# Kernel tuning notes

Hardware: AMD Instinct MI355X
Metric: run time of the kernel (lower is better)

Reference implementation:

```python
import jax, jax.numpy as jnp
import numpy as np

B, C, H, W = 8, 1, 512, 512


def _unwrap(p, axis=-2):
    # Faithful jnp port of np.unwrap (default discont=pi, period=2*pi)
    pi = jnp.pi
    d = jnp.diff(p, axis=axis)
    dd = jnp.mod(d + pi, 2.0 * pi) - pi
    dd = jnp.where((dd == -pi) & (d > 0), pi, dd)
    corr = dd - d
    corr = jnp.where(jnp.abs(d) < pi, 0.0, corr)
    cum = jnp.cumsum(corr, axis=axis)
    pad_cfg = [(0, 0)] * p.ndim
    pad_cfg[axis] = (1, 0)
    return p + jnp.pad(cum, pad_cfg)


def _conv_same(x, w, b, dil):
    # PyTorch padding='same': total = dil*(k-1), left = total//2, right = rest
    th = dil * (w.shape[2] - 1)
    tw = dil * (w.shape[3] - 1)
    pad = [(th // 2, th - th // 2), (tw // 2, tw - tw // 2)]
    y = jax.lax.conv_general_dilated(
        x, w, window_strides=(1, 1), padding=pad,
        rhs_dilation=(dil, dil),
        dimension_numbers=('NCHW', 'OIHW', 'NCHW'))
    return y + b[None, :, None, None]


def setup_inputs() -> dict:
    key = jax.random.key(0)
    ks = jax.random.split(key, 9)
    s = 0.05
    return {
        'feature_in': jax.random.normal(ks[0], (B, C, H, W), dtype=jnp.float32),
        'w1': jax.random.normal(ks[1], (2, 1, 4, 4), dtype=jnp.float32) * s,
        'b1': jax.random.normal(ks[2], (2,), dtype=jnp.float32) * s,
        'w2': jax.random.normal(ks[3], (4, 3, 3, 3), dtype=jnp.float32) * s,
        'b2': jax.random.normal(ks[4], (4,), dtype=jnp.float32) * s,
        'w3': jax.random.normal(ks[5], (8, 8, 2, 2), dtype=jnp.float32) * s,
        'b3': jax.random.normal(ks[6], (8,), dtype=jnp.float32) * s,
        'w4': jax.random.normal(ks[7], (16, 20, 1, 1), dtype=jnp.float32) * s,
        'b4': jax.random.normal(ks[8], (16,), dtype=jnp.float32) * s,
    }


def reference(feature_in, w1, b1, w2, b2, w3, b3, w4, b4):
    out = _unwrap(feature_in, axis=-2)
    diff = out[:, :, 1:, :] - out[:, :, :-1, :]           # [B,C,H-1,W]
    padded = jnp.pad(diff, ((0, 0), (0, 0), (1, 0), (0, 0)))  # pad top of H
    sq = padded * padded                                   # [B,1,H,W]
    o1 = _conv_same(sq, w1, b1, 1)
    o1 = jnp.concatenate((o1, sq), axis=1)                 # 3 ch
    o2 = _conv_same(o1, w2, b2, 2)
    o2 = jnp.concatenate((o2, o1, sq), axis=1)             # 8 ch
    o3 = _conv_same(o2, w3, b3, 3)
    o3 = jnp.concatenate((o3, o2, o1, sq), axis=1)         # 20 ch
    o4 = _conv_same(o3, w4, b4, 4)
    o4 = jnp.concatenate((o4, o3, o2, o1, sq), axis=1)     # 48 ch
    return o4
```

## Files before the change

### kernel.cpp

```cpp
#include <hip/hip_runtime.h>

#define HH 512
#define WW 512
#define TS 32
#define SQH 42
#define SQW 42
#define O1H 39
#define O1W 39
#define O2H 35
#define O2W 35

#define W2T 0
#define W3T 108
#define W4T 332
#define B2O 572
#define B3O 576
#define B4O 584

__global__ void prep_weights(const float* __restrict__ w2, const float* __restrict__ b2,
                             const float* __restrict__ w3, const float* __restrict__ b3,
                             const float* __restrict__ w4, const float* __restrict__ b4,
                             float* __restrict__ ws)
{
    int t = threadIdx.x;
    if (t < 108) {
        int c = t & 3, ci = (t >> 2) % 3, tap = t / 12;
        int i = tap / 3, j = tap % 3;
        ws[W2T + t] = w2[((c*3+ci)*3+i)*3+j];
    }
    if (t < 224) {
        int c = t & 7, ci = (t >> 3) % 7, tap = t / 56;
        int i = tap >> 1, j = tap & 1;
        float v = w3[((c*8+ci)*2+i)*2+j];
        if (ci == 6) v += w3[((c*8+7)*2+i)*2+j];
        ws[W3T + t] = v;
    }
    if (t < 240) {
        int c = t & 15, u = t >> 4;
        float v;
        if (u < 12)       v = w4[c*20+u];
        else if (u == 12) v = w4[c*20+12] + w4[c*20+16];
        else if (u == 13) v = w4[c*20+13] + w4[c*20+17];
        else              v = w4[c*20+14] + w4[c*20+15] + w4[c*20+18] + w4[c*20+19];
        ws[W4T + t] = v;
    }
    if (t < 4)  ws[B2O + t] = b2[t];
    if (t < 8)  ws[B3O + t] = b3[t];
    if (t < 16) ws[B4O + t] = b4[t];
}

__global__ __launch_bounds__(256) void enc_fused(
    const float* __restrict__ f,
    const float* __restrict__ w1, const float* __restrict__ b1,
    const float* __restrict__ wf,
    float* __restrict__ out)
{
    __shared__ __align__(16) float s_sq[SQH*SQW];
    __shared__ __align__(16) float s_o1[O1H*O1W*2];
    __shared__ __align__(16) float s_o2[O2H*O2W*4];

    const int tid = threadIdx.x;
    const int b  = blockIdx.z;
    const int h0 = blockIdx.y * TS;
    const int w0 = blockIdx.x * TS;

    const float* fb = f + (size_t)b * (HH*WW);
    const float PI = 3.14159265358979323846f;
    const float TWO_PI = 6.283185307179586477f;
    #pragma unroll
    for (int p = 0; p < 7; ++p) {
        int idx = tid + 256*p;
        if (idx < SQH*SQW) {
            int rh = idx / SQW, rw = idx % SQW;
            int gh = h0 + rh - 4, gw = w0 + rw - 4;
            float v = 0.f;
            if (gh > 0 && gh < HH && gw >= 0 && gw < WW) {
                float d = fb[gh*WW + gw] - fb[(gh-1)*WW + gw];
                float m = fmodf(d + PI, TWO_PI);
                if (m < 0.f) m += TWO_PI;
                float dd = m - PI;
                if (dd == -PI && d > 0.f) dd = PI;
                float r = (fabsf(d) < PI) ? d : dd;
                v = r * r;
            }
            s_sq[idx] = v;
        }
    }
    __syncthreads();

    #pragma unroll
    for (int p = 0; p < 6; ++p) {
        int idx = tid + 256*p;
        if (idx < O1H*O1W) {
            int rh = idx / O1W, rw = idx % O1W;
            float a0 = b1[0], a1 = b1[1];
            #pragma unroll
            for (int i = 0; i < 4; ++i)
            #pragma unroll
            for (int j = 0; j < 4; ++j) {
                float x = s_sq[(rh+i)*SQW + rw+j];
                a0 += x * w1[i*4+j];
                a1 += x * w1[16+i*4+j];
            }
            int gy = h0 + rh - 3, gx = w0 + rw - 3;
            bool inimg = (gy >= 0) & (gy < HH) & (gx >= 0) & (gx < WW);
            float2 o; o.x = inimg ? a0 : 0.f; o.y = inimg ? a1 : 0.f;
            *(float2*)&s_o1[idx*2] = o;
        }
    }
    __syncthreads();

    {
        int rh[5], rw[5]; bool val[5], img[5];
        float acc[4][5];
        #pragma unroll
        for (int p = 0; p < 5; ++p) {
            int idx = tid + 256*p;
            val[p] = idx < O2H*O2W;
            int id = val[p] ? idx : 0;
            rh[p] = id / O2W; rw[p] = id % O2W;
            int gy = h0 + rh[p] - 1, gx = w0 + rw[p] - 1;
            img[p] = (gy >= 0) & (gy < HH) & (gx >= 0) & (gx < WW);
            #pragma unroll
            for (int c = 0; c < 4; ++c) acc[c][p] = wf[B2O + c];
        }
        #pragma unroll
        for (int i = 0; i < 3; ++i)
        #pragma unroll
        for (int j = 0; j < 3; ++j) {
            const float4 wa = *(const float4*)&wf[W2T + (i*3+j)*12];
            const float4 wb = *(const float4*)&wf[W2T + (i*3+j)*12 + 4];
            const float4 wc = *(const float4*)&wf[W2T + (i*3+j)*12 + 8];
            #pragma unroll
            for (int p = 0; p < 5; ++p) {
                float2 xo = *(const float2*)&s_o1[((rh[p]+2*i)*O1W + rw[p]+2*j)*2];
                float  xs = s_sq[(rh[p]+1+2*i)*SQW + rw[p]+1+2*j];
                acc[0][p] += xo.x*wa.x + xo.y*wb.x + xs*wc.x;
                acc[1][p] += xo.x*wa.y + xo.y*wb.y + xs*wc.y;
                acc[2][p] += xo.x*wa.z + xo.y*wb.z + xs*wc.z;
                acc[3][p] += xo.x*wa.w + xo.y*wb.w + xs*wc.w;
            }
        }
        #pragma unroll
        for (int p = 0; p < 5; ++p) if (val[p]) {
            float4 o;
            o.x = img[p] ? acc[0][p] : 0.f;
            o.y = img[p] ? acc[1][p] : 0.f;
            o.z = img[p] ? acc[2][p] : 0.f;
            o.w = img[p] ? acc[3][p] : 0.f;
            *(float4*)&s_o2[(rh[p]*O2W + rw[p])*4] = o;
        }
    }
    __syncthreads();

    {
        const int rw = tid & 31;
        const int q  = tid >> 5;
        float sqv[4], o1v[2][4], o2v[4][4], o3v[8][4];
        #pragma unroll
        for (int k = 0; k < 4; ++k) {
            int rh = q + 8*k;
            sqv[k] = s_sq[(rh+4)*SQW + rw+4];
            float2 t2 = *(const float2*)&s_o1[((rh+3)*O1W + rw+3)*2];
            o1v[0][k]=t2.x; o1v[1][k]=t2.y;
            float4 t4 = *(const float4*)&s_o2[((rh+1)*O2W + rw+1)*4];
            o2v[0][k]=t4.x; o2v[1][k]=t4.y; o2v[2][k]=t4.z; o2v[3][k]=t4.w;
        }

        const size_t HWp = (size_t)HH*WW;
        float* ob = out + (size_t)b*48*HWp;
        int pofs[4];
        #pragma unroll
        for (int k = 0; k < 4; ++k) pofs[k] = (h0 + q + 8*k)*WW + (w0 + rw);

        #pragma unroll
        for (int k = 0; k < 4; ++k) {
            float* o = ob + pofs[k];
            #pragma unroll
            for (int c = 0; c < 4; ++c) o[(size_t)(24+c)*HWp] = o2v[c][k];
            o[28*HWp]=o1v[0][k]; o[29*HWp]=o1v[1][k]; o[30*HWp]=sqv[k]; o[31*HWp]=sqv[k];
            o[32*HWp]=o1v[0][k]; o[33*HWp]=o1v[1][k]; o[34*HWp]=sqv[k]; o[35*HWp]=sqv[k];
            #pragma unroll
            for (int c = 0; c < 4; ++c) o[(size_t)(36+c)*HWp] = o2v[c][k];
            o[40*HWp]=o1v[0][k]; o[41*HWp]=o1v[1][k]; o[42*HWp]=sqv[k]; o[43*HWp]=sqv[k];
            o[44*HWp]=o1v[0][k]; o[45*HWp]=o1v[1][k]; o[46*HWp]=sqv[k]; o[47*HWp]=sqv[k];
        }

        #pragma unroll
        for (int c = 0; c < 8; ++c) {
            float bv = wf[B3O + c];
            #pragma unroll
            for (int k = 0; k < 4; ++k) o3v[c][k] = bv;
        }
        #pragma unroll
        for (int i = 0; i < 2; ++i)
        #pragma unroll
        for (int j = 0; j < 2; ++j) {
            float xin[7][4];
            #pragma unroll
            for (int k = 0; k < 4; ++k) {
                int hh = q + 8*k + 3*i, ww = rw + 3*j;
                float4 a = *(const float4*)&s_o2[(hh*O2W+ww)*4];
                xin[0][k]=a.x; xin[1][k]=a.y; xin[2][k]=a.z; xin[3][k]=a.w;
                float2 bq = *(const float2*)&s_o1[((hh+2)*O1W + ww+2)*2];
                xin[4][k]=bq.x; xin[5][k]=bq.y;
                xin[6][k]=s_sq[(hh+3)*SQW + ww+3];
            }
            #pragma unroll
            for (int ci = 0; ci < 7; ++ci) {
                float4 wa = *(const float4*)&wf[W3T + (i*2+j)*56 + ci*8];
                float4 wb = *(const float4*)&wf[W3T + (i*2+j)*56 + ci*8 + 4];
                #pragma unroll
                for (int k = 0; k < 4; ++k) {
                    float x = xin[ci][k];
                    o3v[0][k] += x*wa.x; o3v[1][k] += x*wa.y;
                    o3v[2][k] += x*wa.z; o3v[3][k] += x*wa.w;
                    o3v[4][k] += x*wb.x; o3v[5][k] += x*wb.y;
                    o3v[6][k] += x*wb.z; o3v[7][k] += x*wb.w;
                }
            }
        }
        #pragma unroll
        for (int k = 0; k < 4; ++k) {
            float* o = ob + pofs[k];
            #pragma unroll
            for (int c = 0; c < 8; ++c) o[(size_t)(16+c)*HWp] = o3v[c][k];
        }

        #pragma unroll
        for (int cg = 0; cg < 4; ++cg) {
            float acc[4][4];
            #pragma unroll
            for (int c = 0; c < 4; ++c) {
                float bv = wf[B4O + cg*4 + c];
                #pragma unroll
                for (int k = 0; k < 4; ++k) acc[c][k] = bv;
            }
            #pragma unroll
            for (int u = 0; u < 15; ++u) {
                float4 wv = *(const float4*)&wf[W4T + u*16 + cg*4];
                #pragma unroll
                for (int k = 0; k < 4; ++k) {
                    float x = (u<8) ? o3v[u][k] : (u<12) ? o2v[u-8][k]
                            : (u<14) ? o1v[u-12][k] : sqv[k];
                    acc[0][k]+=x*wv.x; acc[1][k]+=x*wv.y;
                    acc[2][k]+=x*wv.z; acc[3][k]+=x*wv.w;
                }
            }
            #pragma unroll
            for (int c = 0; c < 4; ++c)
            #pragma unroll
            for (int k = 0; k < 4; ++k)
                ob[(size_t)(cg*4+c)*HWp + pofs[k]] = acc[c][k];
        }
    }
}

extern "C" void kernel_launch(void* const* d_in, const int* in_sizes, int n_in,
                              void* d_out, int out_size, void* d_ws, size_t ws_size,
                              hipStream_t stream) {
    const float* f  = (const float*)d_in[0];
    const float* w1 = (const float*)d_in[1];
    const float* b1 = (const float*)d_in[2];
    const float* w2 = (const float*)d_in[3];
    const float* b2 = (const float*)d_in[4];
    const float* w3 = (const float*)d_in[5];
    const float* b3 = (const float*)d_in[6];
    const float* w4 = (const float*)d_in[7];
    const float* b4 = (const float*)d_in[8];
    float* out = (float*)d_out;
    float* ws  = (float*)d_ws;

    prep_weights<<<1, 256, 0, stream>>>(w2, b2, w3, b3, w4, b4, ws);
    dim3 grid(WW/TS, HH/TS, 8);
    enc_fused<<<grid, 256, 0, stream>>>(f, w1, b1, ws, out);
}
```

Baseline: 100.4 us.

## Interleave global output stores with compute stages and replace fmodf with floor-based wrap

Output writes for the pass-through sq, o1 and o2 channels now happen right after each stage is computed, before the next barrier, not all at the end. The intent is to spread the large store traffic across the kernel so memory writes overlap with the later conv stages. The phase-wrap fmodf is replaced by an fma with floorf and a reciprocal of two pi, which is cheaper but can differ from fmodf by rounding near the wrap boundaries. Keeping sqv and o1v live across stages may raise register pressure.

```diff
diff --git a/kernel.cpp b/kernel.cpp
--- a/kernel.cpp
+++ b/kernel.cpp
@@ -64,21 +64,28 @@
     const int h0 = blockIdx.y * TS;
     const int w0 = blockIdx.x * TS;
 
+    const int rw = tid & 31;
+    const int q  = tid >> 5;
+    const size_t HWp = (size_t)HH*WW;
+    float* ob = out + (size_t)b*48*HWp;
+    int pofs[4];
+    #pragma unroll
+    for (int k = 0; k < 4; ++k) pofs[k] = (h0 + q + 8*k)*WW + (w0 + rw);
+
     const float* fb = f + (size_t)b * (HH*WW);
     const float PI = 3.14159265358979323846f;
     const float TWO_PI = 6.283185307179586477f;
+    const float INV2PI = 0.15915494309189533577f;
     #pragma unroll
     for (int p = 0; p < 7; ++p) {
         int idx = tid + 256*p;
         if (idx < SQH*SQW) {
-            int rh = idx / SQW, rw = idx % SQW;
-            int gh = h0 + rh - 4, gw = w0 + rw - 4;
+            int rh = idx / SQW, rwp = idx % SQW;
+            int gh = h0 + rh - 4, gw = w0 + rwp - 4;
             float v = 0.f;
             if (gh > 0 && gh < HH && gw >= 0 && gw < WW) {
                 float d = fb[gh*WW + gw] - fb[(gh-1)*WW + gw];
-                float m = fmodf(d + PI, TWO_PI);
-                if (m < 0.f) m += TWO_PI;
-                float dd = m - PI;
+                float dd = fmaf(-TWO_PI, floorf((d + PI) * INV2PI), d);
                 if (dd == -PI && d > 0.f) dd = PI;
                 float r = (fabsf(d) < PI) ? d : dd;
                 v = r * r;
@@ -88,38 +95,56 @@
     }
     __syncthreads();
 
+    float sqv[4];
+    #pragma unroll
+    for (int k = 0; k < 4; ++k) sqv[k] = s_sq[(q + 8*k + 4)*SQW + rw + 4];
+
     #pragma unroll
     for (int p = 0; p < 6; ++p) {
         int idx = tid + 256*p;
         if (idx < O1H*O1W) {
-            int rh = idx / O1W, rw = idx % O1W;
+            int rh = idx / O1W, rwp = idx % O1W;
             float a0 = b1[0], a1 = b1[1];
             #pragma unroll
             for (int i = 0; i < 4; ++i)
             #pragma unroll
             for (int j = 0; j < 4; ++j) {
-                float x = s_sq[(rh+i)*SQW + rw+j];
+                float x = s_sq[(rh+i)*SQW + rwp+j];
                 a0 += x * w1[i*4+j];
                 a1 += x * w1[16+i*4+j];
             }
-            int gy = h0 + rh - 3, gx = w0 + rw - 3;
+            int gy = h0 + rh - 3, gx = w0 + rwp - 3;
             bool inimg = (gy >= 0) & (gy < HH) & (gx >= 0) & (gx < WW);
             float2 o; o.x = inimg ? a0 : 0.f; o.y = inimg ? a1 : 0.f;
             *(float2*)&s_o1[idx*2] = o;
         }
     }
+    #pragma unroll
+    for (int k = 0; k < 4; ++k) {
+        float* o = ob + pofs[k];
+        float v = sqv[k];
+        o[30*HWp]=v; o[31*HWp]=v; o[34*HWp]=v; o[35*HWp]=v;
+        o[42*HWp]=v; o[43*HWp]=v; o[46*HWp]=v; o[47*HWp]=v;
+    }
     __syncthreads();
 
+    float o1v[2][4];
+    #pragma unroll
+    for (int k = 0; k < 4; ++k) {
+        float2 t2 = *(const float2*)&s_o1[((q + 8*k + 3)*O1W + rw + 3)*2];
+        o1v[0][k]=t2.x; o1v[1][k]=t2.y;
+    }
+
     {
-        int rh[5], rw[5]; bool val[5], img[5];
+        int rh[5], rwp[5]; bool val[5], img[5];
         float acc[4][5];
         #pragma unroll
         for (int p = 0; p < 5; ++p) {
             int idx = tid + 256*p;
             val[p] = idx < O2H*O2W;
             int id = val[p] ? idx : 0;
-            rh[p] = id / O2W; rw[p] = id % O2W;
-            int gy = h0 + rh[p] - 1, gx = w0 + rw[p] - 1;
+            rh[p] = id / O2W; rwp[p] = id % O2W;
+            int gy = h0 + rh[p] - 1, gx = w0 + rwp[p] - 1;
             img[p] = (gy >= 0) & (gy < HH) & (gx >= 0) & (gx < WW);
             #pragma unroll
             for (int c = 0; c < 4; ++c) acc[c][p] = wf[B2O + c];
@@ -133,8 +158,8 @@
             const float4 wc = *(const float4*)&wf[W2T + (i*3+j)*12 + 8];
             #pragma unroll
             for (int p = 0; p < 5; ++p) {
-                float2 xo = *(const float2*)&s_o1[((rh[p]+2*i)*O1W + rw[p]+2*j)*2];
-                float  xs = s_sq[(rh[p]+1+2*i)*SQW + rw[p]+1+2*j];
+                float2 xo = *(const float2*)&s_o1[((rh[p]+2*i)*O1W + rwp[p]+2*j)*2];
+                float  xs = s_sq[(rh[p]+1+2*i)*SQW + rwp[p]+1+2*j];
                 acc[0][p] += xo.x*wa.x + xo.y*wb.x + xs*wc.x;
                 acc[1][p] += xo.x*wa.y + xo.y*wb.y + xs*wc.y;
                 acc[2][p] += xo.x*wa.z + xo.y*wb.z + xs*wc.z;
@@ -148,44 +173,27 @@
             o.y = img[p] ? acc[1][p] : 0.f;
             o.z = img[p] ? acc[2][p] : 0.f;
             o.w = img[p] ? acc[3][p] : 0.f;
-            *(float4*)&s_o2[(rh[p]*O2W + rw[p])*4] = o;
-        }
+            *(float4*)&s_o2[(rh[p]*O2W + rwp[p])*4] = o;
+        }
+    }
+    #pragma unroll
+    for (int k = 0; k < 4; ++k) {
+        float* o = ob + pofs[k];
+        float a = o1v[0][k], bb = o1v[1][k];
+        o[28*HWp]=a; o[29*HWp]=bb; o[32*HWp]=a; o[33*HWp]=bb;
+        o[40*HWp]=a; o[41*HWp]=bb; o[44*HWp]=a; o[45*HWp]=bb;
     }
     __syncthreads();
 
+    float o2v[4][4];
+    #pragma unroll
+    for (int k = 0; k < 4; ++k) {
+        float4 t4 = *(const float4*)&s_o2[((q + 8*k + 1)*O2W + rw + 1)*4];
+        o2v[0][k]=t4.x; o2v[1][k]=t4.y; o2v[2][k]=t4.z; o2v[3][k]=t4.w;
+    }
+
     {
-        const int rw = tid & 31;
-        const int q  = tid >> 5;
-        float sqv[4], o1v[2][4], o2v[4][4], o3v[8][4];
-        #pragma unroll
-        for (int k = 0; k < 4; ++k) {
-            int rh = q + 8*k;
-            sqv[k] = s_sq[(rh+4)*SQW + rw+4];
-            float2 t2 = *(const float2*)&s_o1[((rh+3)*O1W + rw+3)*2];
-            o1v[0][k]=t2.x; o1v[1][k]=t2.y;
-            float4 t4 = *(const float4*)&s_o2[((rh+1)*O2W + rw+1)*4];
-            o2v[0][k]=t4.x; o2v[1][k]=t4.y; o2v[2][k]=t4.z; o2v[3][k]=t4.w;
-        }
-
-        const size_t HWp = (size_t)HH*WW;
-        float* ob = out + (size_t)b*48*HWp;
-        int pofs[4];
-        #pragma unroll
-        for (int k = 0; k < 4; ++k) pofs[k] = (h0 + q + 8*k)*WW + (w0 + rw);
-
-        #pragma unroll
-        for (int k = 0; k < 4; ++k) {
-            float* o = ob + pofs[k];
-            #pragma unroll
-            for (int c = 0; c < 4; ++c) o[(size_t)(24+c)*HWp] = o2v[c][k];
-            o[28*HWp]=o1v[0][k]; o[29*HWp]=o1v[1][k]; o[30*HWp]=sqv[k]; o[31*HWp]=sqv[k];
-            o[32*HWp]=o1v[0][k]; o[33*HWp]=o1v[1][k]; o[34*HWp]=sqv[k]; o[35*HWp]=sqv[k];
-            #pragma unroll
-            for (int c = 0; c < 4; ++c) o[(size_t)(36+c)*HWp] = o2v[c][k];
-            o[40*HWp]=o1v[0][k]; o[41*HWp]=o1v[1][k]; o[42*HWp]=sqv[k]; o[43*HWp]=sqv[k];
-            o[44*HWp]=o1v[0][k]; o[45*HWp]=o1v[1][k]; o[46*HWp]=sqv[k]; o[47*HWp]=sqv[k];
-        }
-
+        float o3v[8][4];
         #pragma unroll
         for (int c = 0; c < 8; ++c) {
             float bv = wf[B3O + c];
@@ -224,9 +232,17 @@
         for (int k = 0; k < 4; ++k) {
             float* o = ob + pofs[k];
             #pragma unroll
+            for (int c = 0; c < 4; ++c) {
+                o[(size_t)(24+c)*HWp] = o2v[c][k];
+                o[(size_t)(36+c)*HWp] = o2v[c][k];
+            }
+        }
+        #pragma unroll
+        for (int k = 0; k < 4; ++k) {
+            float* o = ob + pofs[k];
+            #pragma unroll
             for (int c = 0; c < 8; ++c) o[(size_t)(16+c)*HWp] = o3v[c][k];
         }
-
         #pragma unroll
         for (int cg = 0; cg < 4; ++cg) {
             float acc[4][4];
```

Measured after the change: 108.1 us. 7.6% more time.

## Store o2 tile in fp16 shared memory and raise occupancy hint

Applied to the files above, without the earlier changes.

The o2 intermediate in LDS is now stored as half2 pairs instead of float4, roughly halving that buffer so more blocks fit per CU, and launch bounds request 5 blocks per SM. The fmodf-based phase wrap is replaced with a floor/fma formulation. Storing o2 in fp16 loses precision in both the written output channels and the conv3 inputs, which may exceed tolerance. The floor-based wrap can also differ slightly from fmodf at boundaries.

```diff
diff --git a/kernel.cpp b/kernel.cpp
--- a/kernel.cpp
+++ b/kernel.cpp
@@ -1,4 +1,5 @@
 #include <hip/hip_runtime.h>
+#include <hip/hip_fp16.h>
 
 #define HH 512
 #define WW 512
@@ -49,15 +50,15 @@
     if (t < 16) ws[B4O + t] = b4[t];
 }
 
-__global__ __launch_bounds__(256) void enc_fused(
+__global__ __launch_bounds__(256, 5) void enc_fused(
     const float* __restrict__ f,
     const float* __restrict__ w1, const float* __restrict__ b1,
     const float* __restrict__ wf,
     float* __restrict__ out)
 {
-    __shared__ __align__(16) float s_sq[SQH*SQW];
-    __shared__ __align__(16) float s_o1[O1H*O1W*2];
-    __shared__ __align__(16) float s_o2[O2H*O2W*4];
+    __shared__ __align__(16) float   s_sq[SQH*SQW];
+    __shared__ __align__(16) float   s_o1[O1H*O1W*2];
+    __shared__ __align__(16) __half2 s_o2h[O2H*O2W][2];
 
     const int tid = threadIdx.x;
     const int b  = blockIdx.z;
@@ -67,18 +68,17 @@
     const float* fb = f + (size_t)b * (HH*WW);
     const float PI = 3.14159265358979323846f;
     const float TWO_PI = 6.283185307179586477f;
+    const float INV2PI = 0.15915494309189533577f;
     #pragma unroll
     for (int p = 0; p < 7; ++p) {
         int idx = tid + 256*p;
         if (idx < SQH*SQW) {
-            int rh = idx / SQW, rw = idx % SQW;
-            int gh = h0 + rh - 4, gw = w0 + rw - 4;
+            int rh = idx / SQW, rwp = idx % SQW;
+            int gh = h0 + rh - 4, gw = w0 + rwp - 4;
             float v = 0.f;
             if (gh > 0 && gh < HH && gw >= 0 && gw < WW) {
                 float d = fb[gh*WW + gw] - fb[(gh-1)*WW + gw];
-                float m = fmodf(d + PI, TWO_PI);
-                if (m < 0.f) m += TWO_PI;
-                float dd = m - PI;
+                float dd = fmaf(-TWO_PI, floorf((d + PI) * INV2PI), d);
                 if (dd == -PI && d > 0.f) dd = PI;
                 float r = (fabsf(d) < PI) ? d : dd;
                 v = r * r;
@@ -92,17 +92,17 @@
     for (int p = 0; p < 6; ++p) {
         int idx = tid + 256*p;
         if (idx < O1H*O1W) {
-            int rh = idx / O1W, rw = idx % O1W;
+            int rh = idx / O1W, rwp = idx % O1W;
             float a0 = b1[0], a1 = b1[1];
             #pragma unroll
             for (int i = 0; i < 4; ++i)
             #pragma unroll
             for (int j = 0; j < 4; ++j) {
-                float x = s_sq[(rh+i)*SQW + rw+j];
+                float x = s_sq[(rh+i)*SQW + rwp+j];
                 a0 += x * w1[i*4+j];
                 a1 += x * w1[16+i*4+j];
             }
-            int gy = h0 + rh - 3, gx = w0 + rw - 3;
+            int gy = h0 + rh - 3, gx = w0 + rwp - 3;
             bool inimg = (gy >= 0) & (gy < HH) & (gx >= 0) & (gx < WW);
             float2 o; o.x = inimg ? a0 : 0.f; o.y = inimg ? a1 : 0.f;
             *(float2*)&s_o1[idx*2] = o;
@@ -111,15 +111,15 @@
     __syncthreads();
 
     {
-        int rh[5], rw[5]; bool val[5], img[5];
+        int rh[5], rwp[5]; bool val[5], img[5];
         float acc[4][5];
         #pragma unroll
         for (int p = 0; p < 5; ++p) {
             int idx = tid + 256*p;
             val[p] = idx < O2H*O2W;
             int id = val[p] ? idx : 0;
-            rh[p] = id / O2W; rw[p] = id % O2W;
-            int gy = h0 + rh[p] - 1, gx = w0 + rw[p] - 1;
+            rh[p] = id / O2W; rwp[p] = id % O2W;
+            int gy = h0 + rh[p] - 1, gx = w0 + rwp[p] - 1;
             img[p] = (gy >= 0) & (gy < HH) & (gx >= 0) & (gx < WW);
             #pragma unroll
             for (int c = 0; c < 4; ++c) acc[c][p] = wf[B2O + c];
@@ -133,8 +133,8 @@
             const float4 wc = *(const float4*)&wf[W2T + (i*3+j)*12 + 8];
             #pragma unroll
             for (int p = 0; p < 5; ++p) {
-                float2 xo = *(const float2*)&s_o1[((rh[p]+2*i)*O1W + rw[p]+2*j)*2];
-                float  xs = s_sq[(rh[p]+1+2*i)*SQW + rw[p]+1+2*j];
+                float2 xo = *(const float2*)&s_o1[((rh[p]+2*i)*O1W + rwp[p]+2*j)*2];
+                float  xs = s_sq[(rh[p]+1+2*i)*SQW + rwp[p]+1+2*j];
                 acc[0][p] += xo.x*wa.x + xo.y*wb.x + xs*wc.x;
                 acc[1][p] += xo.x*wa.y + xo.y*wb.y + xs*wc.y;
                 acc[2][p] += xo.x*wa.z + xo.y*wb.z + xs*wc.z;
@@ -143,12 +143,13 @@
         }
         #pragma unroll
         for (int p = 0; p < 5; ++p) if (val[p]) {
-            float4 o;
-            o.x = img[p] ? acc[0][p] : 0.f;
-            o.y = img[p] ? acc[1][p] : 0.f;
-            o.z = img[p] ? acc[2][p] : 0.f;
-            o.w = img[p] ? acc[3][p] : 0.f;
-            *(float4*)&s_o2[(rh[p]*O2W + rw[p])*4] = o;
+            float x0 = img[p] ? acc[0][p] : 0.f;
+            float x1 = img[p] ? acc[1][p] : 0.f;
+            float x2 = img[p] ? acc[2][p] : 0.f;
+            float x3 = img[p] ? acc[3][p] : 0.f;
+            int px = rh[p]*O2W + rwp[p];
+            s_o2h[px][0] = __floats2half2_rn(x0, x1);
+            s_o2h[px][1] = __floats2half2_rn(x2, x3);
         }
     }
     __syncthreads();
@@ -156,6 +157,12 @@
     {
         const int rw = tid & 31;
         const int q  = tid >> 5;
+        const size_t HWp = (size_t)HH*WW;
+        float* ob = out + (size_t)b*48*HWp;
+        int pofs[4];
+        #pragma unroll
+        for (int k = 0; k < 4; ++k) pofs[k] = (h0 + q + 8*k)*WW + (w0 + rw);
+
         float sqv[4], o1v[2][4], o2v[4][4], o3v[8][4];
         #pragma unroll
         for (int k = 0; k < 4; ++k) {
@@ -163,15 +170,11 @@
             sqv[k] = s_sq[(rh+4)*SQW + rw+4];
             float2 t2 = *(const float2*)&s_o1[((rh+3)*O1W + rw+3)*2];
             o1v[0][k]=t2.x; o1v[1][k]=t2.y;
-            float4 t4 = *(const float4*)&s_o2[((rh+1)*O2W + rw+1)*4];
-            o2v[0][k]=t4.x; o2v[1][k]=t4.y; o2v[2][k]=t4.z; o2v[3][k]=t4.w;
-        }
-
-        const size_t HWp = (size_t)HH*WW;
-        float* ob = out + (size_t)b*48*HWp;
-        int pofs[4];
-        #pragma unroll
-        for (int k = 0; k < 4; ++k) pofs[k] = (h0 + q + 8*k)*WW + (w0 + rw);
+            int px = (rh+1)*O2W + rw+1;
+            float2 ab = __half22float2(s_o2h[px][0]);
+            float2 cd = __half22float2(s_o2h[px][1]);
+            o2v[0][k]=ab.x; o2v[1][k]=ab.y; o2v[2][k]=cd.x; o2v[3][k]=cd.y;
+        }
 
         #pragma unroll
         for (int k = 0; k < 4; ++k) {
@@ -200,8 +203,10 @@
             #pragma unroll
             for (int k = 0; k < 4; ++k) {
                 int hh = q + 8*k + 3*i, ww = rw + 3*j;
-                float4 a = *(const float4*)&s_o2[(hh*O2W+ww)*4];
-                xin[0][k]=a.x; xin[1][k]=a.y; xin[2][k]=a.z; xin[3][k]=a.w;
+                int px = hh*O2W + ww;
+                float2 ab = __half22float2(s_o2h[px][0]);
+                float2 cd = __half22float2(s_o2h[px][1]);
+                xin[0][k]=ab.x; xin[1][k]=ab.y; xin[2][k]=cd.x; xin[3][k]=cd.y;
                 float2 bq = *(const float2*)&s_o1[((hh+2)*O1W + ww+2)*2];
                 xin[4][k]=bq.x; xin[5][k]=bq.y;
                 xin[6][k]=s_sq[(hh+3)*SQW + ww+3];
```

New measurement: 124.4 us. +23.9%, slower.
